# Performance work log

Hardware: AMD Instinct MI355X
Metric: run time of the kernel (lower is better)

The kernel has to match this reference:

```python
import jax, jax.numpy as jnp
import numpy as np

N_NODES = 100000
N_EDGES = 1600000
NODE_F = 128
EDGE_F = 64
OUT = 32
NEG_SLOPE = 0.01  # torch nn.LeakyReLU default


def setup_inputs() -> dict:
    key = jax.random.key(0)
    ks = jax.random.split(key, 7)
    h = jax.random.normal(ks[0], (N_NODES, NODE_F), dtype=jnp.float32)
    edge_feat = jax.random.normal(ks[1], (N_EDGES, EDGE_F), dtype=jnp.float32)
    src = jax.random.randint(ks[2], (N_EDGES,), 0, N_NODES)
    dst = jax.random.randint(ks[3], (N_EDGES,), 0, N_NODES)
    W_node = jax.random.normal(ks[4], (NODE_F, OUT), dtype=jnp.float32) * 0.05
    W_edge = jax.random.normal(ks[5], (EDGE_F, OUT), dtype=jnp.float32) * 0.05
    attn_w = jax.random.normal(ks[6], (3 * OUT,), dtype=jnp.float32) * 0.05
    return {"h": h, "edge_feat": edge_feat, "src": src, "dst": dst,
            "W_node": W_node, "W_edge": W_edge, "attn_w": attn_w}


def reference(h, edge_feat, src, dst, W_node, W_edge, attn_w):
    # Project node and edge features (bias-free linears).
    z = h @ W_node                      # [N, OUT]
    ez = edge_feat @ W_edge             # [E, OUT]

    # attn_fc on cat(src_z, dst_z, edge_z): split weight vector to avoid
    # materializing the [E, 3*OUT] concat.
    a_src, a_dst, a_edge = attn_w[:OUT], attn_w[OUT:2 * OUT], attn_w[2 * OUT:]
    zs = z[src]                         # [E, OUT] gather
    logits = jax.nn.leaky_relu(
        zs @ a_src + z[dst] @ a_dst + ez @ a_edge, NEG_SLOPE)  # [E]

    # Per-destination (segment) softmax over incoming edges.
    seg_max = jax.ops.segment_max(logits, dst, num_segments=N_NODES)
    seg_max = jnp.where(jnp.isfinite(seg_max), seg_max, 0.0)  # empty segments
    e = jnp.exp(logits - seg_max[dst])                          # [E]
    denom = jax.ops.segment_sum(e, dst, num_segments=N_NODES)  # [N]

    # Weighted sum of src z vectors per destination.
    num = jax.ops.segment_sum(e[:, None] * zs, dst, num_segments=N_NODES)
    u = num / jnp.maximum(denom, 1e-20)[:, None]                # [N, OUT]
    return u
```

## Files before the change

kernel.cpp:

```cpp
#include <hip/hip_runtime.h>
#include <hip/hip_bf16.h>

#define N_NODES 100000
#define N_EDGES 1600000
#define NODE_F 128
#define EDGE_F 64
#define OUT_F 32
#define NEG_SLOPE 0.01f

#define EDGE_BLOCKS 25000
#define PROJ_BLOCKS 12500
#define FUSED_GRID (EDGE_BLOCKS + PROJ_BLOCKS)

__device__ __forceinline__ unsigned short f2bf(float f) {
    unsigned u = __float_as_uint(f);
    unsigned r = u + 0x7fffu + ((u >> 16) & 1u);
    return (unsigned short)(r >> 16);
}
__device__ __forceinline__ float bf2f(unsigned short b) {
    return __uint_as_float((unsigned)b << 16);
}

__global__ __launch_bounds__(256) void k_fused_edge_proj(
    const float* __restrict__ edge_feat,
    const int* __restrict__ dst,
    const float* __restrict__ W_edge,
    const float* __restrict__ h,
    const float* __restrict__ W_node,
    const float* __restrict__ attn_w,
    float* __restrict__ g,
    int* __restrict__ deg,
    unsigned short* __restrict__ zb,
    float* __restrict__ s_src,
    float* __restrict__ s_dst) {
    __shared__ float shmem[NODE_F * OUT_F];

    if (blockIdx.x < EDGE_BLOCKS) {
        float* we_s = shmem;
        if (threadIdx.x < EDGE_F) {
            float a = 0.f;
#pragma unroll
            for (int kk = 0; kk < OUT_F; ++kk)
                a += W_edge[threadIdx.x * OUT_F + kk] * attn_w[2 * OUT_F + kk];
            we_s[threadIdx.x] = a;
        }
        __syncthreads();

        int t = blockIdx.x * 256 + threadIdx.x;
        int e = t >> 2;
        int sub = t & 3;

        const float4* row = (const float4*)(edge_feat + (size_t)e * EDGE_F);
        float acc = 0.f;
#pragma unroll
        for (int i = 0; i < 4; ++i) {
            int fi = sub + i * 4;
            float4 v = row[fi];
            int b = fi * 4;
            acc += v.x * we_s[b] + v.y * we_s[b + 1] + v.z * we_s[b + 2] + v.w * we_s[b + 3];
        }
        acc += __shfl_xor(acc, 1);
        acc += __shfl_xor(acc, 2);

        if (sub == 0) {
            g[e] = acc;
            atomicAdd(deg + dst[e], 1);
        }
    } else {
        float* Ws = shmem;
        for (int i = threadIdx.x; i < NODE_F * OUT_F; i += 256)
            Ws[i] = W_node[i];
        __syncthreads();

        int p = blockIdx.x - EDGE_BLOCKS;
        int node = p * 8 + (threadIdx.x >> 5);
        int o = threadIdx.x & 31;

        const float* hrow = h + (size_t)node * NODE_F;
        float acc = 0.f;
#pragma unroll 8
        for (int j = 0; j < NODE_F; ++j)
            acc += hrow[j] * Ws[j * OUT_F + o];

        zb[(size_t)node * OUT_F + o] = f2bf(acc);

        float ps = acc * attn_w[o];
        float pd = acc * attn_w[OUT_F + o];
#pragma unroll
        for (int m = 16; m >= 1; m >>= 1) {
            ps += __shfl_xor(ps, m, 32);
            pd += __shfl_xor(pd, m, 32);
        }
        if (o == 0) {
            s_src[node] = ps;
            s_dst[node] = pd;
        }
    }
}

__global__ void k_scan_block(const int* __restrict__ deg,
                             int* __restrict__ offs,
                             int* __restrict__ bsum) {
    __shared__ int wsum[4];
    int i = blockIdx.x * 256 + threadIdx.x;
    int lane = threadIdx.x & 63;
    int wid = threadIdx.x >> 6;
    int v = (i < N_NODES) ? deg[i] : 0;
    int x = v;
#pragma unroll
    for (int d = 1; d < 64; d <<= 1) {
        int y = __shfl_up(x, d);
        if (lane >= d) x += y;
    }
    if (lane == 63) wsum[wid] = x;
    __syncthreads();
    int add = 0;
    for (int w = 0; w < wid; ++w) add += wsum[w];
    int incl = x + add;
    if (i < N_NODES) offs[i] = incl - v;
    if (threadIdx.x == 255) bsum[blockIdx.x] = incl;
}

__global__ void k_scan_bsums(int* __restrict__ bsum, int nb) {
    __shared__ int wsum[8];
    int t = threadIdx.x;
    int lane = t & 63;
    int wid = t >> 6;
    int v = (t < nb) ? bsum[t] : 0;
    int x = v;
#pragma unroll
    for (int d = 1; d < 64; d <<= 1) {
        int y = __shfl_up(x, d);
        if (lane >= d) x += y;
    }
    if (lane == 63) wsum[wid] = x;
    __syncthreads();
    int add = 0;
    for (int w = 0; w < wid; ++w) add += wsum[w];
    int incl = x + add;
    if (t < nb) bsum[t] = incl - v;
}

__global__ void k_scan_add(int* __restrict__ offs,
                           const int* __restrict__ bsum,
                           int* __restrict__ cursor) {
    int i = blockIdx.x * 256 + threadIdx.x;
    if (i < N_NODES) {
        int o = offs[i] + bsum[blockIdx.x];
        offs[i] = o;
        cursor[i] = o;
    }
}

__global__ void k_scatter(const int* __restrict__ src,
                          const int* __restrict__ dst,
                          const float* __restrict__ g,
                          const float* __restrict__ s_src,
                          const float* __restrict__ s_dst,
                          int* __restrict__ cursor,
                          int2* __restrict__ perm) {
    int e = blockIdx.x * 256 + threadIdx.x;
    if (e >= N_EDGES) return;
    int s = src[e], d = dst[e];
    float logit = s_src[s] + s_dst[d] + g[e];
    logit = logit > 0.f ? logit : NEG_SLOPE * logit;
    float ev = __expf(logit);
    int pos = atomicAdd(cursor + d, 1);
    perm[pos] = make_int2(s, __float_as_int(ev));
}

__global__ void k_node_aggr(const int* __restrict__ offs,
                            const int* __restrict__ cursor,
                            const int2* __restrict__ perm,
                            const unsigned short* __restrict__ zb,
                            float* __restrict__ out) {
    int node = blockIdx.x * 8 + (threadIdx.x >> 5);
    int k = threadIdx.x & 31;
    if (node >= N_NODES) return;

    int start = offs[node];
    int end = cursor[node];

    float acc = 0.f, den_local = 0.f;
    for (int base = start; base < end; base += 32) {
        int idx = base + k;
        int cnt = min(32, end - base);
        float ev = 0.f;
        int sp = 0;
        if (idx < end) {
            int2 pr = perm[idx];
            sp = pr.x;
            ev = __int_as_float(pr.y);
        }
        den_local += ev;
        int j = 0;
        for (; j + 4 <= cnt; j += 4) {
            float e0 = __shfl(ev, j, 32), e1 = __shfl(ev, j + 1, 32);
            float e2 = __shfl(ev, j + 2, 32), e3 = __shfl(ev, j + 3, 32);
            int s0 = __shfl(sp, j, 32), s1 = __shfl(sp, j + 1, 32);
            int s2 = __shfl(sp, j + 2, 32), s3 = __shfl(sp, j + 3, 32);
            float z0 = bf2f(zb[(size_t)s0 * OUT_F + k]);
            float z1 = bf2f(zb[(size_t)s1 * OUT_F + k]);
            float z2 = bf2f(zb[(size_t)s2 * OUT_F + k]);
            float z3 = bf2f(zb[(size_t)s3 * OUT_F + k]);
            acc += e0 * z0;
            acc += e1 * z1;
            acc += e2 * z2;
            acc += e3 * z3;
        }
        for (; j < cnt; ++j) {
            float evj = __shfl(ev, j, 32);
            int sj = __shfl(sp, j, 32);
            acc += evj * bf2f(zb[(size_t)sj * OUT_F + k]);
        }
    }

    float den = den_local;
#pragma unroll
    for (int msk = 16; msk >= 1; msk >>= 1)
        den += __shfl_xor(den, msk, 32);

    out[(size_t)node * OUT_F + k] =
        (end > start) ? acc / fmaxf(den, 1e-20f) : 0.f;
}

extern "C" void kernel_launch(void* const* d_in, const int* in_sizes, int n_in,
                              void* d_out, int out_size, void* d_ws, size_t ws_size,
                              hipStream_t stream) {
    const float* h         = (const float*)d_in[0];
    const float* edge_feat = (const float*)d_in[1];
    const int*   src       = (const int*)d_in[2];
    const int*   dst       = (const int*)d_in[3];
    const float* W_node    = (const float*)d_in[4];
    const float* W_edge    = (const float*)d_in[5];
    const float* attn_w    = (const float*)d_in[6];
    float* out = (float*)d_out;

    char* ws = (char*)d_ws;
    size_t off = 0;
    auto alloc = [&](size_t bytes) {
        void* p = ws + off;
        off += (bytes + 255) & ~(size_t)255;
        return p;
    };
    unsigned short* zb = (unsigned short*)alloc((size_t)N_NODES * OUT_F * sizeof(unsigned short));
    float* s_src  = (float*)alloc((size_t)N_NODES * sizeof(float));
    float* s_dst  = (float*)alloc((size_t)N_NODES * sizeof(float));
    float* g      = (float*)alloc((size_t)N_EDGES * sizeof(float));
    int*   deg    = (int*)alloc((size_t)N_NODES * sizeof(int));
    int*   offs   = (int*)alloc((size_t)N_NODES * sizeof(int));
    int*   cursor = (int*)alloc((size_t)N_NODES * sizeof(int));
    int*   bsum   = (int*)alloc(1024 * sizeof(int));
    int2*  perm   = (int2*)alloc((size_t)N_EDGES * sizeof(int2));

    const int NB = (N_NODES + 255) / 256;

    hipMemsetAsync(deg, 0, (size_t)N_NODES * sizeof(int), stream);

    k_fused_edge_proj<<<FUSED_GRID, 256, 0, stream>>>(
        edge_feat, dst, W_edge, h, W_node, attn_w, g, deg, zb, s_src, s_dst);

    k_scan_block<<<NB, 256, 0, stream>>>(deg, offs, bsum);
    k_scan_bsums<<<1, 512, 0, stream>>>(bsum, NB);
    k_scan_add<<<NB, 256, 0, stream>>>(offs, bsum, cursor);

    k_scatter<<<(N_EDGES + 255) / 256, 256, 0, stream>>>(
        src, dst, g, s_src, s_dst, cursor, perm);

    k_node_aggr<<<(N_NODES + 7) / 8, 256, 0, stream>>>(
        offs, cursor, perm, zb, out);
}
```

Baseline: 287.5 us.

## Precompute edge attention weights once and coarsen fused edge/projection blocks

Moves the W_edge·attn_edge reduction into a tiny separate kernel, so edge blocks no longer recompute it and no longer need a shared-memory sync. Each edge block now handles 512 edges over 8 passes with weights held in registers. Each projection block handles 16 nodes, two per 32-lane group, with float4 loads of h, which halves how often W_node is loaded into shared memory. The cost is one extra tiny launch and fewer, longer-running blocks.

Result: no change. 291.2 us (+1.3%).

```diff
diff --git a/kernel.cpp b/kernel.cpp
--- a/kernel.cpp
+++ b/kernel.cpp
@@ -8,8 +8,8 @@
 #define OUT_F 32
 #define NEG_SLOPE 0.01f
 
-#define EDGE_BLOCKS 25000
-#define PROJ_BLOCKS 12500
+#define EDGE_BLOCKS 3125
+#define PROJ_BLOCKS 6250
 #define FUSED_GRID (EDGE_BLOCKS + PROJ_BLOCKS)
 
 __device__ __forceinline__ unsigned short f2bf(float f) {
@@ -21,10 +21,21 @@
     return __uint_as_float((unsigned)b << 16);
 }
 
+__global__ void k_edge_w(const float* __restrict__ W_edge,
+                         const float* __restrict__ attn_w,
+                         float* __restrict__ w_e) {
+    int j = threadIdx.x;
+    float acc = 0.f;
+#pragma unroll
+    for (int k = 0; k < OUT_F; ++k)
+        acc += W_edge[j * OUT_F + k] * attn_w[2 * OUT_F + k];
+    w_e[j] = acc;
+}
+
 __global__ __launch_bounds__(256) void k_fused_edge_proj(
     const float* __restrict__ edge_feat,
     const int* __restrict__ dst,
-    const float* __restrict__ W_edge,
+    const float* __restrict__ w_e,
     const float* __restrict__ h,
     const float* __restrict__ W_node,
     const float* __restrict__ attn_w,
@@ -33,67 +44,84 @@
     unsigned short* __restrict__ zb,
     float* __restrict__ s_src,
     float* __restrict__ s_dst) {
-    __shared__ float shmem[NODE_F * OUT_F];
+    __shared__ float Ws[NODE_F * OUT_F];
 
     if (blockIdx.x < EDGE_BLOCKS) {
-        float* we_s = shmem;
-        if (threadIdx.x < EDGE_F) {
-            float a = 0.f;
-#pragma unroll
-            for (int kk = 0; kk < OUT_F; ++kk)
-                a += W_edge[threadIdx.x * OUT_F + kk] * attn_w[2 * OUT_F + kk];
-            we_s[threadIdx.x] = a;
-        }
-        __syncthreads();
-
-        int t = blockIdx.x * 256 + threadIdx.x;
-        int e = t >> 2;
-        int sub = t & 3;
-
-        const float4* row = (const float4*)(edge_feat + (size_t)e * EDGE_F);
-        float acc = 0.f;
-#pragma unroll
-        for (int i = 0; i < 4; ++i) {
-            int fi = sub + i * 4;
-            float4 v = row[fi];
-            int b = fi * 4;
-            acc += v.x * we_s[b] + v.y * we_s[b + 1] + v.z * we_s[b + 2] + v.w * we_s[b + 3];
-        }
-        acc += __shfl_xor(acc, 1);
-        acc += __shfl_xor(acc, 2);
-
-        if (sub == 0) {
-            g[e] = acc;
-            atomicAdd(deg + dst[e], 1);
+        int sub = threadIdx.x & 3;
+        const float4* we4 = (const float4*)w_e;
+        float4 w0 = we4[sub];
+        float4 w1 = we4[sub + 4];
+        float4 w2 = we4[sub + 8];
+        float4 w3 = we4[sub + 12];
+
+        int ebase = blockIdx.x * 512 + (threadIdx.x >> 2);
+#pragma unroll
+        for (int pass = 0; pass < 8; ++pass) {
+            int e = ebase + pass * 64;
+            const float4* row = (const float4*)(edge_feat + (size_t)e * EDGE_F);
+            float4 v0 = row[sub];
+            float4 v1 = row[sub + 4];
+            float4 v2 = row[sub + 8];
+            float4 v3 = row[sub + 12];
+            float acc = v0.x * w0.x + v0.y * w0.y + v0.z * w0.z + v0.w * w0.w;
+            acc += v1.x * w1.x + v1.y * w1.y + v1.z * w1.z + v1.w * w1.w;
+            acc += v2.x * w2.x + v2.y * w2.y + v2.z * w2.z + v2.w * w2.w;
+            acc += v3.x * w3.x + v3.y * w3.y + v3.z * w3.z + v3.w * w3.w;
+            acc += __shfl_xor(acc, 1);
+            acc += __shfl_xor(acc, 2);
+            if (sub == 0) {
+                g[e] = acc;
+                atomicAdd(deg + dst[e], 1);
+            }
         }
     } else {
-        float* Ws = shmem;
         for (int i = threadIdx.x; i < NODE_F * OUT_F; i += 256)
             Ws[i] = W_node[i];
         __syncthreads();
 
         int p = blockIdx.x - EDGE_BLOCKS;
-        int node = p * 8 + (threadIdx.x >> 5);
+        int grp = threadIdx.x >> 5;
         int o = threadIdx.x & 31;
-
-        const float* hrow = h + (size_t)node * NODE_F;
-        float acc = 0.f;
+        int n0 = p * 16 + grp * 2;
+        int n1 = n0 + 1;
+
+        float aw_s = attn_w[o];
+        float aw_d = attn_w[OUT_F + o];
+
+        const float4* h0 = (const float4*)(h + (size_t)n0 * NODE_F);
+        const float4* h1 = (const float4*)(h + (size_t)n1 * NODE_F);
+
+        float a0 = 0.f, a1 = 0.f;
 #pragma unroll 8
-        for (int j = 0; j < NODE_F; ++j)
-            acc += hrow[j] * Ws[j * OUT_F + o];
-
-        zb[(size_t)node * OUT_F + o] = f2bf(acc);
-
-        float ps = acc * attn_w[o];
-        float pd = acc * attn_w[OUT_F + o];
+        for (int j4 = 0; j4 < NODE_F / 4; ++j4) {
+            float4 v0 = h0[j4];
+            float4 v1 = h1[j4];
+            int jb = j4 * 4;
+            float ws0 = Ws[(jb + 0) * OUT_F + o];
+            float ws1 = Ws[(jb + 1) * OUT_F + o];
+            float ws2 = Ws[(jb + 2) * OUT_F + o];
+            float ws3 = Ws[(jb + 3) * OUT_F + o];
+            a0 += v0.x * ws0 + v0.y * ws1 + v0.z * ws2 + v0.w * ws3;
+            a1 += v1.x * ws0 + v1.y * ws1 + v1.z * ws2 + v1.w * ws3;
+        }
+
+        zb[(size_t)n0 * OUT_F + o] = f2bf(a0);
+        zb[(size_t)n1 * OUT_F + o] = f2bf(a1);
+
+        float ps0 = a0 * aw_s, pd0 = a0 * aw_d;
+        float ps1 = a1 * aw_s, pd1 = a1 * aw_d;
 #pragma unroll
         for (int m = 16; m >= 1; m >>= 1) {
-            ps += __shfl_xor(ps, m, 32);
-            pd += __shfl_xor(pd, m, 32);
+            ps0 += __shfl_xor(ps0, m, 32);
+            pd0 += __shfl_xor(pd0, m, 32);
+            ps1 += __shfl_xor(ps1, m, 32);
+            pd1 += __shfl_xor(pd1, m, 32);
         }
         if (o == 0) {
-            s_src[node] = ps;
-            s_dst[node] = pd;
+            s_src[n0] = ps0;
+            s_dst[n0] = pd0;
+            s_src[n1] = ps1;
+            s_dst[n1] = pd1;
         }
     }
 }
@@ -247,6 +275,7 @@
     float* s_src  = (float*)alloc((size_t)N_NODES * sizeof(float));
     float* s_dst  = (float*)alloc((size_t)N_NODES * sizeof(float));
     float* g      = (float*)alloc((size_t)N_EDGES * sizeof(float));
+    float* w_e    = (float*)alloc(EDGE_F * sizeof(float));
     int*   deg    = (int*)alloc((size_t)N_NODES * sizeof(int));
     int*   offs   = (int*)alloc((size_t)N_NODES * sizeof(int));
     int*   cursor = (int*)alloc((size_t)N_NODES * sizeof(int));
@@ -257,8 +286,10 @@
 
     hipMemsetAsync(deg, 0, (size_t)N_NODES * sizeof(int), stream);
 
+    k_edge_w<<<1, 64, 0, stream>>>(W_edge, attn_w, w_e);
+
     k_fused_edge_proj<<<FUSED_GRID, 256, 0, stream>>>(
-        edge_feat, dst, W_edge, h, W_node, attn_w, g, deg, zb, s_src, s_dst);
+        edge_feat, dst, w_e, h, W_node, attn_w, g, deg, zb, s_src, s_dst);
 
     k_scan_block<<<NB, 256, 0, stream>>>(deg, offs, bsum);
     k_scan_bsums<<<1, 512, 0, stream>>>(bsum, NB);
```
